# Kernel tuning notes

Hardware: AMD Instinct MI355X
Metric: run time of the kernel (lower is better)

## Reference

```python
import jax, jax.numpy as jnp
import numpy as np

TEMPLATE_SZ = 7
MAX_SR = 3


def setup_inputs() -> dict:
    key = jax.random.key(0)
    # image-like values in [0, 255) since the module ends with a uint8 cast
    x = jax.random.uniform(key, (2, 1, 192, 192), dtype=jnp.float32) * 255.0
    return {"inputs": x, "search_range": 3}


def reference(inputs, search_range):
    # Equivalent math to: pad(max_sr) -> unfold(k, pad=k//2) -> unfold(s) ->
    # permute -> slice sub-window -> reshape -> uint8.
    # Both zero-pads commute, so fold them into one pad and gather directly,
    # avoiding the huge duplicated double-im2col intermediate.
    k = TEMPLATE_SZ
    max_sr = MAX_SR
    cv = 2 * search_range + 1          # cost_volume_sz
    offset = max_sr - search_range
    B, C, H, W = inputs.shape          # C == 1 (implied by the torch view)
    pad = max_sr + k // 2              # combined zero padding
    Q = jnp.pad(inputs[:, 0].astype(jnp.float32), ((0, 0), (pad, pad), (pad, pad)))
    r = offset + jnp.arange(cv)        # search offsets within max window
    t = jnp.arange(k)                  # template offsets
    # windows[b,i,j,dy,dx,ty,tx] = Q[b, i + r[dy] + ty, j + r[dx] + tx]
    iy = jnp.arange(H)[:, None, None] + r[None, :, None] + t[None, None, :]  # [H, cv, k]
    jx = jnp.arange(W)[:, None, None] + r[None, :, None] + t[None, None, :]  # [W, cv, k]
    win = Q[:, iy[:, None, :, None, :, None], jx[None, :, None, :, None, :]]  # [B,H,W,cv,cv,k,k]
    return win.reshape(B, H, W, cv * cv, k * k).astype(jnp.uint8)
```

## Files before the change

kernel.cpp:

```cpp
#include <hip/hip_runtime.h>


#define KT 7
#define K2 49
#define MAX_SR 3
#define B_ 2
#define H_ 192
#define W_ 192
#define PAD 6
#define PX 48
#define PCOLS (PX + 2*PAD)
#define PSTRIDE 61
#define PROWS 13
#define NTHREADS 256

typedef int vint4 __attribute__((ext_vector_type(4)));

__global__ __launch_bounds__(NTHREADS) void esw_kernel(
    const float* __restrict__ in, int* __restrict__ out,
    int cv, int offset, int d )
{
    __shared__ int patch[PROWS * PSTRIDE];
    __shared__ unsigned short tbl[K2 * K2];

    const int tid = threadIdx.x;
    const int w0 = blockIdx.x * PX;
    const int h  = blockIdx.y;
    const int b  = blockIdx.z;

    const float* inb = in + b * (H_ * W_);
    for (int i = tid; i < PROWS * PCOLS; i += NTHREADS) {
        int dy = i / PCOLS;
        int dx = i - dy * PCOLS;
        int y = h + dy - PAD;
        int x = w0 + dx - PAD;
        int v = 0;
        if ((unsigned)y < (unsigned)H_ && (unsigned)x < (unsigned)W_)
            v = (int)inb[y * W_ + x];
        patch[dy * PSTRIDE + dx] = v;
    }
    for (int j = tid; j < d; j += NTHREADS) {
        int rr = j / K2;
        int tt = j - rr * K2;
        int ry = rr / cv;
        int rx = rr - ry * cv;
        int ty = tt / KT;
        int tx = tt - ty * KT;
        tbl[j] = (unsigned short)((offset + ry + ty) * PSTRIDE + (offset + rx + tx));
    }
    __syncthreads();

    const int total = PX * d;
    long long p0 = (long long)(b * H_ + h) * W_ + w0;
    int* outp = out + p0 * d;

    int g = 4 * tid;
    int j = g, p = 0;
    while (j >= d) { j -= d; ++p; }
    for (; g < total; g += 4 * NTHREADS) {
        if (j + 3 < d) {
            vint4 v;
            v.x = patch[tbl[j]     + p];
            v.y = patch[tbl[j + 1] + p];
            v.z = patch[tbl[j + 2] + p];
            v.w = patch[tbl[j + 3] + p];
            __builtin_nontemporal_store(v, (vint4*)(outp + g));
        } else {
            #pragma unroll
            for (int u = 0; u < 4; ++u) {
                int jj = j + u, pp = p;
                if (jj >= d) { jj -= d; ++pp; }
                __builtin_nontemporal_store(patch[tbl[jj] + pp], outp + g + u);
            }
        }
        j += 4 * NTHREADS;
        while (j >= d) { j -= d; ++p; }
    }
}

extern "C" void kernel_launch(void* const* d_in, const int* in_sizes, int n_in,
                              void* d_out, int out_size, void* d_ws, size_t ws_size,
                              hipStream_t stream) {
    const float* in = (const float*)d_in[0];
    int* out = (int*)d_out;

    int cv2 = out_size / (B_ * H_ * W_ * K2);
    int cv = 1;
    while (cv * cv < cv2) ++cv;
    int offset = MAX_SR - (cv - 1) / 2;
    int d = cv2 * K2;

    dim3 grid(W_ / PX, H_, B_);
    esw_kernel<<<grid, NTHREADS, 0, stream>>>(in, out, cv, offset, d);
}
```

Measured before the change: 716.9 us.

## Precompute per-thread gather offsets in registers, drop shared index table

Replaces the shared-memory index table and the per-iteration modular index stepping with offsets held in registers. Each thread computes the 40 patch offsets for its fixed position within a 4-pixel group once. The main loop then walks 12 groups of 4 output pixels, adding a constant pixel shift, so no index decode or extra LDS lookup is done in the hot loop. This costs a large register array (RMAX=10 by 4), which may lower occupancy, and it assumes d is at most 2560 for correctness.

Measured after the change: 741.8 us. 3.5% more time.

```diff
diff --git a/kernel.cpp b/kernel.cpp
--- a/kernel.cpp
+++ b/kernel.cpp
@@ -13,6 +13,7 @@
 #define PSTRIDE 61
 #define PROWS 13
 #define NTHREADS 256
+#define RMAX 10
 
 typedef int vint4 __attribute__((ext_vector_type(4)));
 
@@ -21,7 +22,6 @@
     int cv, int offset, int d )
 {
     __shared__ int patch[PROWS * PSTRIDE];
-    __shared__ unsigned short tbl[K2 * K2];
 
     const int tid = threadIdx.x;
     const int w0 = blockIdx.x * PX;
@@ -39,42 +39,47 @@
             v = (int)inb[y * W_ + x];
         patch[dy * PSTRIDE + dx] = v;
     }
-    for (int j = tid; j < d; j += NTHREADS) {
-        int rr = j / K2;
-        int tt = j - rr * K2;
-        int ry = rr / cv;
-        int rx = rr - ry * cv;
-        int ty = tt / KT;
-        int tx = tt - ty * KT;
-        tbl[j] = (unsigned short)((offset + ry + ty) * PSTRIDE + (offset + rx + tx));
+
+    int e[RMAX][4];
+    #pragma unroll
+    for (int r = 0; r < RMAX; ++r) {
+        int q = tid + NTHREADS * r;
+        int j4 = 4 * q;
+        #pragma unroll
+        for (int u = 0; u < 4; ++u) {
+            int jj = j4 + u;
+            if (jj >= 4 * d) jj = 4 * d - 1;
+            int p_in = jj / d;
+            int j  = jj - p_in * d;
+            int rr = j / K2;
+            int tt = j - rr * K2;
+            int ry = rr / cv;
+            int rx = rr - ry * cv;
+            int ty = tt / KT;
+            int tx = tt - ty * KT;
+            e[r][u] = (offset + ry + ty) * PSTRIDE + (offset + rx + tx) + p_in;
+        }
     }
     __syncthreads();
 
-    const int total = PX * d;
     long long p0 = (long long)(b * H_ + h) * W_ + w0;
-    int* outp = out + p0 * d;
+    int* op = out + p0 * (long long)d;
 
-    int g = 4 * tid;
-    int j = g, p = 0;
-    while (j >= d) { j -= d; ++p; }
-    for (; g < total; g += 4 * NTHREADS) {
-        if (j + 3 < d) {
-            vint4 v;
-            v.x = patch[tbl[j]     + p];
-            v.y = patch[tbl[j + 1] + p];
-            v.z = patch[tbl[j + 2] + p];
-            v.w = patch[tbl[j + 3] + p];
-            __builtin_nontemporal_store(v, (vint4*)(outp + g));
-        } else {
-            #pragma unroll
-            for (int u = 0; u < 4; ++u) {
-                int jj = j + u, pp = p;
-                if (jj >= d) { jj -= d; ++pp; }
-                __builtin_nontemporal_store(patch[tbl[jj] + pp], outp + g + u);
+    for (int gidx = 0; gidx < PX / 4; ++gidx) {
+        const int pb = 4 * gidx;
+        #pragma unroll
+        for (int r = 0; r < RMAX; ++r) {
+            int q = tid + NTHREADS * r;
+            if (q < d) {
+                vint4 v;
+                v.x = patch[e[r][0] + pb];
+                v.y = patch[e[r][1] + pb];
+                v.z = patch[e[r][2] + pb];
+                v.w = patch[e[r][3] + pb];
+                __builtin_nontemporal_store(v, (vint4*)(op + 4 * q));
             }
         }
-        j += 4 * NTHREADS;
-        while (j >= d) { j -= d; ++p; }
+        op += 4 * d;
     }
 }
 
```

## Use persistent 1024-thread blocks with whole padded image in LDS as bytes

Applied to the files above, without the earlier changes.

Replaces the per-row 48-pixel tile grid with 512 persistent blocks of 1024 threads. Each block loads its batch's entire zero-padded image into shared memory as uint8 and strides over 4096-element output chunks, using a precomputed magic multiplier instead of a running divide to find the pixel index. This drops redundant halo loads and the serial wrap loop, and swaps nontemporal stores for plain vector stores. In exchange every block reloads the full image (about 41KB of LDS), which limits occupancy and adds startup cost per block.

After: 712.6 us. No clear change (-0.6%).

```diff
diff --git a/kernel.cpp b/kernel.cpp
--- a/kernel.cpp
+++ b/kernel.cpp
@@ -7,37 +7,35 @@
 #define B_ 2
 #define H_ 192
 #define W_ 192
+#define HW (H_ * W_)
 #define PAD 6
-#define PX 48
-#define PCOLS (PX + 2*PAD)
-#define PSTRIDE 61
-#define PROWS 13
-#define NTHREADS 256
+#define PY 204
+#define PIMG (PY * PY)
+#define NTHREADS 1024
+#define NB 512
 
 typedef int vint4 __attribute__((ext_vector_type(4)));
 
 __global__ __launch_bounds__(NTHREADS) void esw_kernel(
     const float* __restrict__ in, int* __restrict__ out,
-    int cv, int offset, int d )
+    int cv, int offset, int d , unsigned long long M )
 {
-    __shared__ int patch[PROWS * PSTRIDE];
+    __shared__ unsigned char pimg[PIMG];
     __shared__ unsigned short tbl[K2 * K2];
 
     const int tid = threadIdx.x;
-    const int w0 = blockIdx.x * PX;
-    const int h  = blockIdx.y;
-    const int b  = blockIdx.z;
+    const int bid = blockIdx.x;
+    const int batch = bid >> 8;
 
-    const float* inb = in + b * (H_ * W_);
-    for (int i = tid; i < PROWS * PCOLS; i += NTHREADS) {
-        int dy = i / PCOLS;
-        int dx = i - dy * PCOLS;
-        int y = h + dy - PAD;
-        int x = w0 + dx - PAD;
-        int v = 0;
-        if ((unsigned)y < (unsigned)H_ && (unsigned)x < (unsigned)W_)
-            v = (int)inb[y * W_ + x];
-        patch[dy * PSTRIDE + dx] = v;
+    const float* inb = in + batch * HW;
+    for (int i = tid; i < PIMG; i += NTHREADS) {
+        int y = i / PY;
+        int x = i - y * PY;
+        int yy = y - PAD, xx = x - PAD;
+        unsigned char v = 0;
+        if ((unsigned)yy < (unsigned)H_ && (unsigned)xx < (unsigned)W_)
+            v = (unsigned char)(int)inb[yy * W_ + xx];
+        pimg[i] = v;
     }
     for (int j = tid; j < d; j += NTHREADS) {
         int rr = j / K2;
@@ -46,35 +44,38 @@
         int rx = rr - ry * cv;
         int ty = tt / KT;
         int tx = tt - ty * KT;
-        tbl[j] = (unsigned short)((offset + ry + ty) * PSTRIDE + (offset + rx + tx));
+        tbl[j] = (unsigned short)((offset + ry + ty) * PY + (offset + rx + tx));
     }
     __syncthreads();
 
-    const int total = PX * d;
-    long long p0 = (long long)(b * H_ + h) * W_ + w0;
-    int* outp = out + p0 * d;
-
-    int g = 4 * tid;
-    int j = g, p = 0;
-    while (j >= d) { j -= d; ++p; }
-    for (; g < total; g += 4 * NTHREADS) {
+    const int nchunk = 9 * d;
+    const unsigned cb = (unsigned)batch * (unsigned)nchunk;
+    const int bathw = batch * HW;
+    for (unsigned c = (unsigned)(bid & 255); c < (unsigned)nchunk; c += 256u) {
+        unsigned J = ((cb + c) << 12) + 4u * (unsigned)tid;
+        unsigned p = (unsigned)(((unsigned long long)J * M) >> 45);
+        int j = (int)(J - p * (unsigned)d);
+        int pr = (int)p - bathw;
+        int h = pr / W_;
+        int w = pr - h * W_;
+        int base = h * PY + w;
         if (j + 3 < d) {
             vint4 v;
-            v.x = patch[tbl[j]     + p];
-            v.y = patch[tbl[j + 1] + p];
-            v.z = patch[tbl[j + 2] + p];
-            v.w = patch[tbl[j + 3] + p];
-            __builtin_nontemporal_store(v, (vint4*)(outp + g));
+            v.x = (int)pimg[base + tbl[j]];
+            v.y = (int)pimg[base + tbl[j + 1]];
+            v.z = (int)pimg[base + tbl[j + 2]];
+            v.w = (int)pimg[base + tbl[j + 3]];
+            *(vint4*)(out + J) = v;
         } else {
             #pragma unroll
             for (int u = 0; u < 4; ++u) {
-                int jj = j + u, pp = p;
-                if (jj >= d) { jj -= d; ++pp; }
-                __builtin_nontemporal_store(patch[tbl[jj] + pp], outp + g + u);
+                int jj = j + u, pr2 = pr;
+                if (jj >= d) { jj -= d; ++pr2; }
+                int h2 = pr2 / W_;
+                int w2 = pr2 - h2 * W_;
+                out[J + u] = (int)pimg[h2 * PY + w2 + tbl[jj]];
             }
         }
-        j += 4 * NTHREADS;
-        while (j >= d) { j -= d; ++p; }
     }
 }
 
@@ -89,7 +90,7 @@
     while (cv * cv < cv2) ++cv;
     int offset = MAX_SR - (cv - 1) / 2;
     int d = cv2 * K2;
+    unsigned long long M = ((1ULL << 45) + (unsigned long long)d - 1) / (unsigned long long)d;
 
-    dim3 grid(W_ / PX, H_, B_);
-    esw_kernel<<<grid, NTHREADS, 0, stream>>>(in, out, cv, offset, d);
+    esw_kernel<<<NB, NTHREADS, 0, stream>>>(in, out, cv, offset, d, M);
 }
```
